# Kernel optimization log

Hardware: AMD Instinct MI355X
Metric: run time of the kernel (lower is better)

## Reference

```python
import jax, jax.numpy as jnp
import numpy as np

V, E, H, T = 100000, 256, 256, 8192


def setup_inputs() -> dict:
    key = jax.random.key(0)
    k0, k1, k2, k3, k4, k5 = jax.random.split(key, 6)
    s = 1.0 / np.sqrt(H)  # PyTorch LSTM init bound
    tokens = jax.random.randint(k0, (T,), 0, V)
    embedding = jax.random.normal(k1, (V, E), jnp.float32) * 0.02
    W_ih = jax.random.uniform(k2, (4 * H, E), jnp.float32, -s, s)
    W_hh = jax.random.uniform(k3, (4 * H, H), jnp.float32, -s, s)
    b_ih = jax.random.uniform(k4, (4 * H,), jnp.float32, -s, s)
    b_hh = jax.random.uniform(k5, (4 * H,), jnp.float32, -s, s)
    return {"tokens": tokens, "embedding": embedding, "W_ih": W_ih,
            "W_hh": W_hh, "b_ih": b_ih, "b_hh": b_hh}


def reference(tokens, embedding, W_ih, W_hh, b_ih, b_hh):
    # Flattened tree traversal: one embed + one LSTM cell step per token,
    # hidden state threaded through, all per-token hiddens collected.
    emb = embedding[tokens]                      # [T, E] gather (memory-bound)
    # precompute input contribution for every step (batched GEMM)
    xg = emb @ W_ih.T + (b_ih + b_hh)            # [T, 4H]

    def step(carry, xg_t):
        h, c = carry
        g = xg_t + W_hh @ h                      # [4H]
        i, f, gg, o = jnp.split(g, 4)
        i = jax.nn.sigmoid(i)
        f = jax.nn.sigmoid(f)
        gg = jnp.tanh(gg)
        o = jax.nn.sigmoid(o)
        c = f * c + i * gg
        h = o * jnp.tanh(c)
        return (h, c), h

    h0 = jnp.zeros((H,), emb.dtype)
    c0 = jnp.zeros((H,), emb.dtype)
    (h_last, c_last), hiddens = jax.lax.scan(step, (h0, c0), xg)
    return hiddens, h_last, c_last
```

## Files before the change

### kernel.cpp

```cpp
#include <hip/hip_runtime.h>
#include <hip/hip_bf16.h>

#define T_STEPS 8192
#define HID 256
#define NWG 16
#define THREADS 256

__device__ __forceinline__ float sigm(float x) { return 1.0f / (1.0f + __expf(-x)); }
__device__ __forceinline__ float tanh_fast(float x) { return 2.0f / (1.0f + __expf(-2.0f * x)) - 1.0f; }

__global__ __launch_bounds__(THREADS, 1)
void lstm_scan(const int* __restrict__ tokens,
               const float* __restrict__ emb,
               const float* __restrict__ Wih,
               const float* __restrict__ Whh,
               const float* __restrict__ bih,
               const float* __restrict__ bhh,
               float* __restrict__ out,
               unsigned long long* __restrict__ hbuf)
{
    const int tid  = threadIdx.x;
    const int w    = blockIdx.x;
    const int lane = tid & 63;
    const int wave = tid >> 6;
    const int rl   = lane >> 2;
    const int kq   = lane & 3;
    const int r_wg = wave * 16 + rl;
    const int unit_local = r_wg >> 2;
    const int gate = r_wg & 3;
    const int unit = w * 16 + unit_local;
    const int grow = gate * 256 + unit;
    const int kbase = kq * 64;

    float whh[64], wih[64];
    {
        const float* p = Whh + (size_t)grow * 256 + kbase;
        #pragma unroll
        for (int j = 0; j < 64; j += 4) {
            float4 q = *(const float4*)(p + j);
            whh[j] = q.x; whh[j+1] = q.y; whh[j+2] = q.z; whh[j+3] = q.w;
        }
        p = Wih + (size_t)grow * 256 + kbase;
        #pragma unroll
        for (int j = 0; j < 64; j += 4) {
            float4 q = *(const float4*)(p + j);
            wih[j] = q.x; wih[j+1] = q.y; wih[j+2] = q.z; wih[j+3] = q.w;
        }
    }
    const float bias = bih[grow] + bhh[grow];
    const bool owner = ((lane & 15) == 0);

    __shared__ float4 lds_h4[4][17];
    __shared__ float4 lds_e4[2][4][17];

    if (owner)
        __hip_atomic_store(hbuf + unit, 0ull, __ATOMIC_RELAXED, __HIP_MEMORY_SCOPE_AGENT);
    if (wave == 1) {
        int tk = tokens[0];
        float4 e = *(const float4*)(emb + (size_t)tk * 256 + lane * 4);
        lds_e4[0][lane >> 4][lane & 15] = e;
    }
    float c = 0.0f;
    const float act_scale = (gate == 2) ? 2.0f : 1.0f;
    const float act_off   = (gate == 2) ? 1.0f : 0.0f;
    __syncthreads();

    for (int t = 0; t < T_STEPS; ++t) {
        if (wave == 1) {
            int tk = tokens[(t + 1 < T_STEPS) ? t + 1 : t];
            float4 e = *(const float4*)(emb + (size_t)tk * 256 + lane * 4);
            lds_e4[(t + 1) & 1][lane >> 4][lane & 15] = e;
        }
        float acc = 0.0f;
        {
            const float4* eb = lds_e4[t & 1][kq];
            #pragma unroll
            for (int i = 0; i < 16; ++i) {
                float4 v = eb[i];
                acc = fmaf(wih[4*i+0], v.x, acc);
                acc = fmaf(wih[4*i+1], v.y, acc);
                acc = fmaf(wih[4*i+2], v.z, acc);
                acc = fmaf(wih[4*i+3], v.w, acc);
            }
        }
        if (wave == 0) {
            const unsigned long long* hb = hbuf + (size_t)(t & 1) * 256 + lane * 4;
            unsigned long long p0, p1, p2, p3;
            const unsigned int tt = (unsigned int)t;
            for (;;) {
                p0 = __hip_atomic_load(hb + 0, __ATOMIC_RELAXED, __HIP_MEMORY_SCOPE_AGENT);
                p1 = __hip_atomic_load(hb + 1, __ATOMIC_RELAXED, __HIP_MEMORY_SCOPE_AGENT);
                p2 = __hip_atomic_load(hb + 2, __ATOMIC_RELAXED, __HIP_MEMORY_SCOPE_AGENT);
                p3 = __hip_atomic_load(hb + 3, __ATOMIC_RELAXED, __HIP_MEMORY_SCOPE_AGENT);
                if ((unsigned int)(p0 >> 32) == tt && (unsigned int)(p1 >> 32) == tt &&
                    (unsigned int)(p2 >> 32) == tt && (unsigned int)(p3 >> 32) == tt)
                    break;
            }
            union { unsigned int i; float f; } a, b, cc, d;
            a.i = (unsigned int)p0; b.i = (unsigned int)p1;
            cc.i = (unsigned int)p2; d.i = (unsigned int)p3;
            lds_h4[lane >> 4][lane & 15] = make_float4(a.f, b.f, cc.f, d.f);
        }
        __syncthreads();
        {
            const float4* hb4 = lds_h4[kq];
            #pragma unroll
            for (int i = 0; i < 16; ++i) {
                float4 v = hb4[i];
                acc = fmaf(whh[4*i+0], v.x, acc);
                acc = fmaf(whh[4*i+1], v.y, acc);
                acc = fmaf(whh[4*i+2], v.z, acc);
                acc = fmaf(whh[4*i+3], v.w, acc);
            }
        }
        acc += __shfl_xor(acc, 1, 64);
        acc += __shfl_xor(acc, 2, 64);
        acc += bias;
        float e  = __expf(-act_scale * acc);
        float av = act_scale / (1.0f + e) - act_off;
        const int base = lane & 48;
        float fv = __shfl(av, base + 4,  64);
        float gv = __shfl(av, base + 8,  64);
        float ov = __shfl(av, base + 12, 64);
        if (owner) {
            c = fmaf(fv, c, av * gv);
            float h = ov * tanh_fast(c);
            union { unsigned int i; float f; } u; u.f = h;
            unsigned long long pk =
                (((unsigned long long)(unsigned int)(t + 1)) << 32) | (unsigned long long)u.i;
            __hip_atomic_store(hbuf + (size_t)((t + 1) & 1) * 256 + unit, pk,
                               __ATOMIC_RELAXED, __HIP_MEMORY_SCOPE_AGENT);
            out[(size_t)t * HID + unit] = h;
            if (t == T_STEPS - 1) {
                out[(size_t)T_STEPS * HID + unit]       = h;
                out[(size_t)T_STEPS * HID + HID + unit] = c;
            }
        }
    }
}

extern "C" void kernel_launch(void* const* d_in, const int* in_sizes, int n_in,
                              void* d_out, int out_size, void* d_ws, size_t ws_size,
                              hipStream_t stream) {
    const int*   tokens = (const int*)d_in[0];
    const float* emb    = (const float*)d_in[1];
    const float* Wih    = (const float*)d_in[2];
    const float* Whh    = (const float*)d_in[3];
    const float* bih    = (const float*)d_in[4];
    const float* bhh    = (const float*)d_in[5];
    float* out = (float*)d_out;
    unsigned long long* hbuf = (unsigned long long*)d_ws;

    lstm_scan<<<NWG, THREADS, 0, stream>>>(tokens, emb, Wih, Whh, bih, bhh, out, hbuf);
}
```

Measured before the change: 12.71 ms.

## Split LSTM scan into 64 single-wave workgroups without block barriers

```diff
diff --git a/kernel.cpp b/kernel.cpp
--- a/kernel.cpp
+++ b/kernel.cpp
@@ -1,12 +1,10 @@
 #include <hip/hip_runtime.h>
-#include <hip/hip_bf16.h>
 
 #define T_STEPS 8192
 #define HID 256
-#define NWG 16
-#define THREADS 256
+#define NWG 64
+#define THREADS 64
 
-__device__ __forceinline__ float sigm(float x) { return 1.0f / (1.0f + __expf(-x)); }
 __device__ __forceinline__ float tanh_fast(float x) { return 2.0f / (1.0f + __expf(-2.0f * x)) - 1.0f; }
 
 __global__ __launch_bounds__(THREADS, 1)
@@ -19,16 +17,13 @@
                float* __restrict__ out,
                unsigned long long* __restrict__ hbuf)
 {
-    const int tid  = threadIdx.x;
+    const int lane = threadIdx.x;
     const int w    = blockIdx.x;
-    const int lane = tid & 63;
-    const int wave = tid >> 6;
-    const int rl   = lane >> 2;
     const int kq   = lane & 3;
-    const int r_wg = wave * 16 + rl;
-    const int unit_local = r_wg >> 2;
-    const int gate = r_wg & 3;
-    const int unit = w * 16 + unit_local;
+    const int r    = lane >> 2;
+    const int gate = r & 3;
+    const int ul   = r >> 2;
+    const int unit = w * 4 + ul;
     const int grow = gate * 256 + unit;
     const int kbase = kq * 64;
 
@@ -49,75 +44,83 @@
     }
     const float bias = bih[grow] + bhh[grow];
     const bool owner = ((lane & 15) == 0);
+    const float act_scale = (gate == 2) ? 2.0f : 1.0f;
+    const float act_off   = (gate == 2) ? 1.0f : 0.0f;
 
-    __shared__ float4 lds_h4[4][17];
-    __shared__ float4 lds_e4[2][4][17];
+    __shared__ float4 lds_h[4][17];
+    __shared__ float4 lds_e[4][17];
 
     if (owner)
         __hip_atomic_store(hbuf + unit, 0ull, __ATOMIC_RELAXED, __HIP_MEMORY_SCOPE_AGENT);
-    if (wave == 1) {
-        int tk = tokens[0];
-        float4 e = *(const float4*)(emb + (size_t)tk * 256 + lane * 4);
-        lds_e4[0][lane >> 4][lane & 15] = e;
+    {
+        int tk0 = tokens[0];
+        lds_e[lane >> 4][lane & 15] = *(const float4*)(emb + (size_t)tk0 * 256 + lane * 4);
     }
+    int tk_next = tokens[1];
     float c = 0.0f;
-    const float act_scale = (gate == 2) ? 2.0f : 1.0f;
-    const float act_off   = (gate == 2) ? 1.0f : 0.0f;
-    __syncthreads();
 
     for (int t = 0; t < T_STEPS; ++t) {
-        if (wave == 1) {
-            int tk = tokens[(t + 1 < T_STEPS) ? t + 1 : t];
-            float4 e = *(const float4*)(emb + (size_t)tk * 256 + lane * 4);
-            lds_e4[(t + 1) & 1][lane >> 4][lane & 15] = e;
-        }
-        float acc = 0.0f;
+        float4 ereg = *(const float4*)(emb + (size_t)tk_next * 256 + lane * 4);
+        int tk_nn = tokens[(t + 2 < T_STEPS) ? t + 2 : T_STEPS - 1];
+
+        float aA = 0.0f, aB = 0.0f, aC = 0.0f, aD = 0.0f;
         {
-            const float4* eb = lds_e4[t & 1][kq];
+            const float4* eb = lds_e[kq];
             #pragma unroll
-            for (int i = 0; i < 16; ++i) {
-                float4 v = eb[i];
-                acc = fmaf(wih[4*i+0], v.x, acc);
-                acc = fmaf(wih[4*i+1], v.y, acc);
-                acc = fmaf(wih[4*i+2], v.z, acc);
-                acc = fmaf(wih[4*i+3], v.w, acc);
+            for (int i = 0; i < 16; i += 4) {
+                float4 v0 = eb[i], v1 = eb[i+1], v2 = eb[i+2], v3 = eb[i+3];
+                aA = fmaf(wih[4*i+ 0], v0.x, aA); aA = fmaf(wih[4*i+ 1], v0.y, aA);
+                aA = fmaf(wih[4*i+ 2], v0.z, aA); aA = fmaf(wih[4*i+ 3], v0.w, aA);
+                aB = fmaf(wih[4*i+ 4], v1.x, aB); aB = fmaf(wih[4*i+ 5], v1.y, aB);
+                aB = fmaf(wih[4*i+ 6], v1.z, aB); aB = fmaf(wih[4*i+ 7], v1.w, aB);
+                aC = fmaf(wih[4*i+ 8], v2.x, aC); aC = fmaf(wih[4*i+ 9], v2.y, aC);
+                aC = fmaf(wih[4*i+10], v2.z, aC); aC = fmaf(wih[4*i+11], v2.w, aC);
+                aD = fmaf(wih[4*i+12], v3.x, aD); aD = fmaf(wih[4*i+13], v3.y, aD);
+                aD = fmaf(wih[4*i+14], v3.z, aD); aD = fmaf(wih[4*i+15], v3.w, aD);
             }
         }
-        if (wave == 0) {
+
+        unsigned long long p0, p1, p2, p3;
+        {
             const unsigned long long* hb = hbuf + (size_t)(t & 1) * 256 + lane * 4;
-            unsigned long long p0, p1, p2, p3;
             const unsigned int tt = (unsigned int)t;
             for (;;) {
                 p0 = __hip_atomic_load(hb + 0, __ATOMIC_RELAXED, __HIP_MEMORY_SCOPE_AGENT);
                 p1 = __hip_atomic_load(hb + 1, __ATOMIC_RELAXED, __HIP_MEMORY_SCOPE_AGENT);
                 p2 = __hip_atomic_load(hb + 2, __ATOMIC_RELAXED, __HIP_MEMORY_SCOPE_AGENT);
                 p3 = __hip_atomic_load(hb + 3, __ATOMIC_RELAXED, __HIP_MEMORY_SCOPE_AGENT);
-                if ((unsigned int)(p0 >> 32) == tt && (unsigned int)(p1 >> 32) == tt &&
-                    (unsigned int)(p2 >> 32) == tt && (unsigned int)(p3 >> 32) == tt)
+                if (((unsigned int)(p0 >> 32) == tt) & ((unsigned int)(p1 >> 32) == tt) &
+                    ((unsigned int)(p2 >> 32) == tt) & ((unsigned int)(p3 >> 32) == tt))
                     break;
             }
-            union { unsigned int i; float f; } a, b, cc, d;
-            a.i = (unsigned int)p0; b.i = (unsigned int)p1;
-            cc.i = (unsigned int)p2; d.i = (unsigned int)p3;
-            lds_h4[lane >> 4][lane & 15] = make_float4(a.f, b.f, cc.f, d.f);
         }
-        __syncthreads();
         {
-            const float4* hb4 = lds_h4[kq];
+            union { unsigned int i; float f; } ha, hb_, hc, hd;
+            ha.i = (unsigned int)p0; hb_.i = (unsigned int)p1;
+            hc.i = (unsigned int)p2; hd.i = (unsigned int)p3;
+            lds_h[lane >> 4][lane & 15] = make_float4(ha.f, hb_.f, hc.f, hd.f);
+        }
+        {
+            const float4* hq = lds_h[kq];
             #pragma unroll
-            for (int i = 0; i < 16; ++i) {
-                float4 v = hb4[i];
-                acc = fmaf(whh[4*i+0], v.x, acc);
-                acc = fmaf(whh[4*i+1], v.y, acc);
-                acc = fmaf(whh[4*i+2], v.z, acc);
-                acc = fmaf(whh[4*i+3], v.w, acc);
+            for (int i = 0; i < 16; i += 4) {
+                float4 v0 = hq[i], v1 = hq[i+1], v2 = hq[i+2], v3 = hq[i+3];
+                aA = fmaf(whh[4*i+ 0], v0.x, aA); aA = fmaf(whh[4*i+ 1], v0.y, aA);
+                aA = fmaf(whh[4*i+ 2], v0.z, aA); aA = fmaf(whh[4*i+ 3], v0.w, aA);
+                aB = fmaf(whh[4*i+ 4], v1.x, aB); aB = fmaf(whh[4*i+ 5], v1.y, aB);
+                aB = fmaf(whh[4*i+ 6], v1.z, aB); aB = fmaf(whh[4*i+ 7], v1.w, aB);
+                aC = fmaf(whh[4*i+ 8], v2.x, aC); aC = fmaf(whh[4*i+ 9], v2.y, aC);
+                aC = fmaf(whh[4*i+10], v2.z, aC); aC = fmaf(whh[4*i+11], v2.w, aC);
+                aD = fmaf(whh[4*i+12], v3.x, aD); aD = fmaf(whh[4*i+13], v3.y, aD);
+                aD = fmaf(whh[4*i+14], v3.z, aD); aD = fmaf(whh[4*i+15], v3.w, aD);
             }
         }
+        float acc = (aA + aB) + (aC + aD);
         acc += __shfl_xor(acc, 1, 64);
         acc += __shfl_xor(acc, 2, 64);
         acc += bias;
-        float e  = __expf(-act_scale * acc);
-        float av = act_scale / (1.0f + e) - act_off;
+        float ex = __expf(-act_scale * acc);
+        float av = act_scale / (1.0f + ex) - act_off;
         const int base = lane & 48;
         float fv = __shfl(av, base + 4,  64);
         float gv = __shfl(av, base + 8,  64);
@@ -136,6 +139,8 @@
                 out[(size_t)T_STEPS * HID + HID + unit] = c;
             }
         }
+        lds_e[lane >> 4][lane & 15] = ereg;
+        tk_next = tk_nn;
     }
 }
 
```

Result: slower. 14.36 ms (+13.0%).

## Co-locate recurrent workgroups on one XCD and exchange hidden state via L2

Applied to the files above, without the earlier changes.

```diff
diff --git a/kernel.cpp b/kernel.cpp
--- a/kernel.cpp
+++ b/kernel.cpp
@@ -1,13 +1,31 @@
 #include <hip/hip_runtime.h>
-#include <hip/hip_bf16.h>
 
 #define T_STEPS 8192
 #define HID 256
-#define NWG 16
+#define NBLK 128
 #define THREADS 256
-
-__device__ __forceinline__ float sigm(float x) { return 1.0f / (1.0f + __expf(-x)); }
+#define SPIN_MAX 4096
+
+#define MAGIC_READY 0x13579BDFu
+#define EMPTY_XCD   0xFFFFFFFFu
+
 __device__ __forceinline__ float tanh_fast(float x) { return 2.0f / (1.0f + __expf(-2.0f * x)) - 1.0f; }
+
+__device__ __forceinline__ void st_u64_sc0(unsigned long long* p, unsigned long long v) {
+    asm volatile("global_store_dwordx2 %0, %1, off sc0" :: "v"(p), "v"(v) : "memory");
+}
+__device__ __forceinline__ void ld4_u64_sc0(const unsigned long long* p,
+                                            unsigned long long& a, unsigned long long& b,
+                                            unsigned long long& c, unsigned long long& d) {
+    asm volatile(
+        "global_load_dwordx2 %0, %4, off sc0\n\t"
+        "global_load_dwordx2 %1, %4, off offset:8 sc0\n\t"
+        "global_load_dwordx2 %2, %4, off offset:16 sc0\n\t"
+        "global_load_dwordx2 %3, %4, off offset:24 sc0\n\t"
+        "s_waitcnt vmcnt(0)"
+        : "=&v"(a), "=&v"(b), "=&v"(c), "=&v"(d)
+        : "v"(p) : "memory");
+}
 
 __global__ __launch_bounds__(THREADS, 1)
 void lstm_scan(const int* __restrict__ tokens,
@@ -17,10 +35,41 @@
                const float* __restrict__ bih,
                const float* __restrict__ bhh,
                float* __restrict__ out,
-               unsigned long long* __restrict__ hbuf)
+               unsigned long long* __restrict__ hbL,
+               unsigned long long* __restrict__ hbA,
+               unsigned* __restrict__ ctl)
 {
+    __shared__ int s_role;
+    if (threadIdx.x == 0) {
+        unsigned xcc;
+        asm volatile("s_getreg_b32 %0, hwreg(HW_REG_XCC_ID, 0, 4)" : "=s"(xcc));
+        unsigned* ready   = ctl + 0;
+        unsigned* elected = ctl + 1;
+        unsigned* cnt     = ctl + 2;
+        if (blockIdx.x == 0) {
+            for (int i = 0; i < 8; ++i)
+                __hip_atomic_store(cnt + i, 0u, __ATOMIC_RELAXED, __HIP_MEMORY_SCOPE_AGENT);
+            __hip_atomic_store(elected, EMPTY_XCD, __ATOMIC_RELAXED, __HIP_MEMORY_SCOPE_AGENT);
+            __hip_atomic_store(ready, MAGIC_READY, __ATOMIC_RELEASE, __HIP_MEMORY_SCOPE_AGENT);
+        }
+        while (__hip_atomic_load(ready, __ATOMIC_ACQUIRE, __HIP_MEMORY_SCOPE_AGENT) != MAGIC_READY)
+            asm volatile("s_sleep 1");
+        unsigned r = __hip_atomic_fetch_add(cnt + xcc, 1u, __ATOMIC_RELAXED, __HIP_MEMORY_SCOPE_AGENT);
+        if (r == 15u) {
+            unsigned expv = EMPTY_XCD;
+            __hip_atomic_compare_exchange_strong(elected, &expv, xcc,
+                __ATOMIC_RELAXED, __ATOMIC_RELAXED, __HIP_MEMORY_SCOPE_AGENT);
+        }
+        unsigned e;
+        while ((e = __hip_atomic_load(elected, __ATOMIC_ACQUIRE, __HIP_MEMORY_SCOPE_AGENT)) == EMPTY_XCD)
+            asm volatile("s_sleep 1");
+        s_role = (xcc == e && r < 16u) ? (int)r : -1;
+    }
+    __syncthreads();
+    const int w = s_role;
+    if (w < 0) return;
+
     const int tid  = threadIdx.x;
-    const int w    = blockIdx.x;
     const int lane = tid & 63;
     const int wave = tid >> 6;
     const int rl   = lane >> 2;
@@ -49,20 +98,23 @@
     }
     const float bias = bih[grow] + bhh[grow];
     const bool owner = ((lane & 15) == 0);
+    const float act_scale = (gate == 2) ? 2.0f : 1.0f;
+    const float act_off   = (gate == 2) ? 1.0f : 0.0f;
 
     __shared__ float4 lds_h4[4][17];
     __shared__ float4 lds_e4[2][4][17];
 
-    if (owner)
-        __hip_atomic_store(hbuf + unit, 0ull, __ATOMIC_RELAXED, __HIP_MEMORY_SCOPE_AGENT);
+    if (owner) {
+        st_u64_sc0(hbL + unit, 0ull);
+        __hip_atomic_store(hbA + unit, 0ull, __ATOMIC_RELAXED, __HIP_MEMORY_SCOPE_AGENT);
+    }
     if (wave == 1) {
         int tk = tokens[0];
         float4 e = *(const float4*)(emb + (size_t)tk * 256 + lane * 4);
         lds_e4[0][lane >> 4][lane & 15] = e;
     }
     float c = 0.0f;
-    const float act_scale = (gate == 2) ? 2.0f : 1.0f;
-    const float act_off   = (gate == 2) ? 1.0f : 0.0f;
+    bool useL2 = true;
     __syncthreads();
 
     for (int t = 0; t < T_STEPS; ++t) {
@@ -84,17 +136,33 @@
             }
         }
         if (wave == 0) {
-            const unsigned long long* hb = hbuf + (size_t)(t & 1) * 256 + lane * 4;
+            const size_t po = (size_t)(t & 1) * 256 + lane * 4;
             unsigned long long p0, p1, p2, p3;
             const unsigned int tt = (unsigned int)t;
-            for (;;) {
-                p0 = __hip_atomic_load(hb + 0, __ATOMIC_RELAXED, __HIP_MEMORY_SCOPE_AGENT);
-                p1 = __hip_atomic_load(hb + 1, __ATOMIC_RELAXED, __HIP_MEMORY_SCOPE_AGENT);
-                p2 = __hip_atomic_load(hb + 2, __ATOMIC_RELAXED, __HIP_MEMORY_SCOPE_AGENT);
-                p3 = __hip_atomic_load(hb + 3, __ATOMIC_RELAXED, __HIP_MEMORY_SCOPE_AGENT);
-                if ((unsigned int)(p0 >> 32) == tt && (unsigned int)(p1 >> 32) == tt &&
-                    (unsigned int)(p2 >> 32) == tt && (unsigned int)(p3 >> 32) == tt)
-                    break;
+            bool got = false;
+            if (useL2) {
+                const unsigned long long* hb = hbL + po;
+                int n = 0;
+                for (;;) {
+                    ld4_u64_sc0(hb, p0, p1, p2, p3);
+                    if (((unsigned int)(p0 >> 32) == tt) & ((unsigned int)(p1 >> 32) == tt) &
+                        ((unsigned int)(p2 >> 32) == tt) & ((unsigned int)(p3 >> 32) == tt)) {
+                        got = true; break;
+                    }
+                    if (++n > SPIN_MAX) { useL2 = false; break; }
+                }
+            }
+            if (!got) {
+                const unsigned long long* hb = hbA + po;
+                for (;;) {
+                    p0 = __hip_atomic_load(hb + 0, __ATOMIC_RELAXED, __HIP_MEMORY_SCOPE_AGENT);
+                    p1 = __hip_atomic_load(hb + 1, __ATOMIC_RELAXED, __HIP_MEMORY_SCOPE_AGENT);
+                    p2 = __hip_atomic_load(hb + 2, __ATOMIC_RELAXED, __HIP_MEMORY_SCOPE_AGENT);
+                    p3 = __hip_atomic_load(hb + 3, __ATOMIC_RELAXED, __HIP_MEMORY_SCOPE_AGENT);
+                    if (((unsigned int)(p0 >> 32) == tt) & ((unsigned int)(p1 >> 32) == tt) &
+                        ((unsigned int)(p2 >> 32) == tt) & ((unsigned int)(p3 >> 32) == tt))
+                        break;
+                }
             }
             union { unsigned int i; float f; } a, b, cc, d;
             a.i = (unsigned int)p0; b.i = (unsigned int)p1;
@@ -116,8 +184,8 @@
         acc += __shfl_xor(acc, 1, 64);
         acc += __shfl_xor(acc, 2, 64);
         acc += bias;
-        float e  = __expf(-act_scale * acc);
-        float av = act_scale / (1.0f + e) - act_off;
+        float ex = __expf(-act_scale * acc);
+        float av = act_scale / (1.0f + ex) - act_off;
         const int base = lane & 48;
         float fv = __shfl(av, base + 4,  64);
         float gv = __shfl(av, base + 8,  64);
@@ -128,8 +196,10 @@
             union { unsigned int i; float f; } u; u.f = h;
             unsigned long long pk =
                 (((unsigned long long)(unsigned int)(t + 1)) << 32) | (unsigned long long)u.i;
-            __hip_atomic_store(hbuf + (size_t)((t + 1) & 1) * 256 + unit, pk,
-                               __ATOMIC_RELAXED, __HIP_MEMORY_SCOPE_AGENT);
+            const size_t so = (size_t)((t + 1) & 1) * 256 + unit;
+            st_u64_sc0(hbL + so, pk);
+            __hip_atomic_store(hbA + so, pk, __ATOMIC_RELAXED,
+                               __HIP_MEMORY_SCOPE_AGENT);
             out[(size_t)t * HID + unit] = h;
             if (t == T_STEPS - 1) {
                 out[(size_t)T_STEPS * HID + unit]       = h;
@@ -137,6 +207,9 @@
             }
         }
     }
+
+    if (w == 0 && tid == 0)
+        __hip_atomic_store(ctl + 0, 0u, __ATOMIC_RELAXED, __HIP_MEMORY_SCOPE_AGENT);
 }
 
 extern "C" void kernel_launch(void* const* d_in, const int* in_sizes, int n_in,
@@ -149,7 +222,9 @@
     const float* bih    = (const float*)d_in[4];
     const float* bhh    = (const float*)d_in[5];
     float* out = (float*)d_out;
-    unsigned long long* hbuf = (unsigned long long*)d_ws;
-
-    lstm_scan<<<NWG, THREADS, 0, stream>>>(tokens, emb, Wih, Whh, bih, bhh, out, hbuf);
-}
+    unsigned long long* hbL = (unsigned long long*)d_ws;
+    unsigned long long* hbA = (unsigned long long*)((char*)d_ws + 4096);
+    unsigned* ctl = (unsigned*)((char*)d_ws + 8192);
+
+    lstm_scan<<<NBLK, THREADS, 0, stream>>>(tokens, emb, Wih, Whh, bih, bhh, out, hbL, hbA, ctl);
+}
```

Result: no change. 12.59 ms (-0.9%).
